# Optimization experiments

Hardware: AMD Instinct MI355X
Metric: run time of the kernel (lower is better)

The kernel has to match this reference:

```python
import jax, jax.numpy as jnp
import numpy as np

N_HEAD, D_MODEL, D_HEAD = 16, 1024, 64
SCALE = 1.0 / (D_HEAD ** 0.5)
LN_EPS = 1e-5


def _rel_shift(x):
    # x: [b, n, i, j] -> Transformer-XL relative shift
    b, n, i, j = x.shape
    zero_pad = jnp.zeros((b, n, i, 1), x.dtype)
    x_padded = jnp.concatenate([zero_pad, x], axis=3).reshape(b, n, j + 1, i)
    return x_padded[:, :, 1:, :].reshape(b, n, i, j)


def setup_inputs() -> dict:
    key = jax.random.key(0)
    ks = jax.random.split(key, 16)
    qlen, bsz, mem_len = 1024, 2, 1024
    klen = qlen + mem_len
    rlen = klen
    s = 0.02
    inp = {
        'w': jax.random.normal(ks[0], (qlen, bsz, D_MODEL), jnp.float32),
        'r': jax.random.normal(ks[1], (rlen, D_MODEL), jnp.float32),
        'mems': jax.random.normal(ks[2], (mem_len, bsz, D_MODEL), jnp.float32),
        'r_w_bias': s * jax.random.normal(ks[3], (N_HEAD, D_HEAD), jnp.float32),
        'r_r_bias': s * jax.random.normal(ks[4], (N_HEAD, D_HEAD), jnp.float32),
        # causal mask with memory offset: position i attends to j <= i + mem_len
        'attn_mask': jnp.triu(jnp.ones((qlen, klen), bool), k=1 + mem_len),
        'Wq': s * jax.random.normal(ks[5], (D_MODEL, N_HEAD * D_HEAD), jnp.float32),
        'bq': jnp.zeros((N_HEAD * D_HEAD,), jnp.float32),
        'Wk': s * jax.random.normal(ks[6], (D_MODEL, N_HEAD * D_HEAD), jnp.float32),
        'bk': jnp.zeros((N_HEAD * D_HEAD,), jnp.float32),
        'Wv': s * jax.random.normal(ks[7], (D_MODEL, N_HEAD * D_HEAD), jnp.float32),
        'bv': jnp.zeros((N_HEAD * D_HEAD,), jnp.float32),
        'Wr': s * jax.random.normal(ks[8], (D_MODEL, N_HEAD * D_HEAD), jnp.float32),
        'br': jnp.zeros((N_HEAD * D_HEAD,), jnp.float32),
        'Wo': s * jax.random.normal(ks[9], (N_HEAD * D_HEAD, D_MODEL), jnp.float32),
        'bo': jnp.zeros((D_MODEL,), jnp.float32),
        'ln_g': jnp.ones((D_MODEL,), jnp.float32),
        'ln_b': jnp.zeros((D_MODEL,), jnp.float32),
    }
    return inp


def reference(w, r, mems, r_w_bias, r_r_bias, Wq, bq, Wk, bk, Wv, bv, Wr, br, Wo, bo, ln_g, ln_b, attn_mask):
    qlen, bsz, _ = w.shape
    cat = jnp.concatenate([mems, w], axis=0)                      # [klen, b, d_model]
    klen = cat.shape[0]
    q = (cat @ Wq + bq)[-qlen:].reshape(qlen, bsz, N_HEAD, D_HEAD)
    k = (cat @ Wk + bk).reshape(klen, bsz, N_HEAD, D_HEAD)
    v = (cat @ Wv + bv).reshape(klen, bsz, N_HEAD, D_HEAD)
    rk = (r @ Wr + br).reshape(-1, N_HEAD, D_HEAD)               # [rlen, n, d]

    AC = jnp.einsum('ibnd,jbnd->bnij', q + r_w_bias, k)          # content term
    BD = _rel_shift(jnp.einsum('ibnd,jnd->bnij', q + r_r_bias, rk))  # relative term
    attn_score = SCALE * (AC + BD)                                # [b, n, i, j]
    attn_score = jnp.where(attn_mask[None, None, :, :], -jnp.inf, attn_score)
    attn_prob = jax.nn.softmax(attn_score, axis=3)
    attn_vec = jnp.einsum('bnij,jbnd->ibnd', attn_prob, v).reshape(qlen, bsz, N_HEAD * D_HEAD)
    attn_out = attn_vec @ Wo + bo

    res = w + attn_out                                            # post-LN (pre_lnorm=False)
    mu = jnp.mean(res, axis=-1, keepdims=True)
    var = jnp.var(res, axis=-1, keepdims=True)
    return (res - mu) / jnp.sqrt(var + LN_EPS) * ln_g + ln_b
```

## Files before the change

kernel.cpp:

```cpp
#include <hip/hip_runtime.h>
#include <math.h>

#define N_HEADC 16
#define D_MODELC 1024
#define D_HEADC 64
#define QLENC 1024
#define BSZC 2
#define MEMLENC 1024
#define KLENC 2048
#define SCALEC 0.125f
#define SL2C 0.18033688011112042f
#define LN_EPSC 1e-5f
#define RINGC 192

typedef __attribute__((ext_vector_type(8))) short short8;
typedef __attribute__((ext_vector_type(4))) float f32x4;

#define MFMA16(a, b, c) __builtin_amdgcn_mfma_f32_16x16x32_bf16((a), (b), (c), 0, 0, 0)

__device__ inline unsigned short f2bf(float x) {
    union { float f; unsigned int u; } c; c.f = x;
    unsigned int r = c.u + 0x7FFFu + ((c.u >> 16) & 1u);
    return (unsigned short)(r >> 16);
}
__device__ inline unsigned int pk2(float a, float b) {
    union { float f; unsigned int u; } x, y; x.f = a; y.f = b;
    return (x.u >> 16) | (y.u & 0xFFFF0000u);
}
__device__ inline float bf2f(short s) {
    union { unsigned int u; float f; } c; c.u = ((unsigned int)(unsigned short)s) << 16;
    return c.f;
}

__device__ __forceinline__ void load_lds16(const short* g, short* l) {
    __builtin_amdgcn_global_load_lds(
        (const __attribute__((address_space(1))) void*)g,
        (__attribute__((address_space(3))) void*)l,
        16, 0, 0);
}

__global__ __launch_bounds__(256) void cast_cat_kernel(
    const float* __restrict__ s0, const float* __restrict__ s1, int splitElems,
    short* __restrict__ dst)
{
    int idx = (blockIdx.x * 256 + threadIdx.x) * 8;
    const float* src = (idx < splitElems) ? (s0 + idx) : (s1 + (idx - splitElems));
    short8 o;
    #pragma unroll
    for (int e = 0; e < 8; ++e) o[e] = (short)f2bf(src[e]);
    *(short8*)(dst + idx) = o;
}

__global__ __launch_bounds__(256) void tcast5_kernel(
    const float* __restrict__ W0, const float* __restrict__ W1,
    const float* __restrict__ W2, const float* __restrict__ W3,
    const float* __restrict__ W4,
    short* __restrict__ D0, short* __restrict__ D1, short* __restrict__ D2,
    short* __restrict__ D3, short* __restrict__ D4)
{
    __shared__ short tile[64][72];
    const float* W; short* D;
    switch (blockIdx.z) {
        case 0: W = W0; D = D0; break;
        case 1: W = W1; D = D1; break;
        case 2: W = W2; D = D2; break;
        case 3: W = W3; D = D3; break;
        default: W = W4; D = D4; break;
    }
    const int t = threadIdx.x;
    const int n0 = blockIdx.x * 64, k0 = blockIdx.y * 64;
    #pragma unroll
    for (int it = 0; it < 2; ++it) {
        int idx = t + it * 256;
        int kl = idx >> 3, c8 = idx & 7;
        const float* src = W + (size_t)(k0 + kl) * D_MODELC + n0 + c8 * 8;
        short8 s;
        #pragma unroll
        for (int e = 0; e < 8; ++e) s[e] = (short)f2bf(src[e]);
        *(short8*)&tile[kl][c8 * 8] = s;
    }
    __syncthreads();
    #pragma unroll
    for (int it = 0; it < 2; ++it) {
        int idx = t + it * 256;
        int nl = idx >> 3, c8 = idx & 7;
        short8 s;
        #pragma unroll
        for (int e = 0; e < 8; ++e) s[e] = tile[c8 * 8 + e][nl];
        *(short8*)(D + (size_t)(n0 + nl) * D_MODELC + k0 + c8 * 8) = s;
    }
}

__global__ __launch_bounds__(256) void vtrans_kernel(
    const short* __restrict__ v_bf, short* __restrict__ vt)
{
    __shared__ short tile[64][72];
    const int t = threadIdx.x;
    const int j0 = blockIdx.x * 64;
    const int bn = blockIdx.y;
    const int b = bn & 1, n = bn >> 1;
    #pragma unroll
    for (int it = 0; it < 2; ++it) {
        int idx = t + it * 256;
        int jl = idx >> 3, c8 = idx & 7;
        short8 s = *(const short8*)(v_bf + ((size_t)(j0 + jl) * 2 + b) * D_MODELC + n * 64 + c8 * 8);
        *(short8*)&tile[jl][c8 * 8] = s;
    }
    __syncthreads();
    #pragma unroll
    for (int it = 0; it < 2; ++it) {
        int idx = t + it * 256;
        int dl = idx >> 3, c8 = idx & 7;
        short8 s;
        #pragma unroll
        for (int e = 0; e < 8; ++e) s[e] = tile[c8 * 8 + e][dl];
        *(short8*)(vt + ((size_t)(b * 16 + n) * 64 + dl) * (size_t)KLENC + j0 + c8 * 8) = s;
    }
}

__global__ __launch_bounds__(256, 3) void proj_gemm_kernel(
    const short* __restrict__ cat, const short* __restrict__ rin,
    const short* __restrict__ WqT, const short* __restrict__ WkT,
    const short* __restrict__ WvT, const short* __restrict__ WrT,
    const float* __restrict__ bq, const float* __restrict__ bk,
    const float* __restrict__ bv, const float* __restrict__ br,
    const float* __restrict__ rwb, const float* __restrict__ rrb,
    short* __restrict__ qw, short* __restrict__ qr,
    short* __restrict__ kb, short* __restrict__ vb, short* __restrict__ rk)
{
    __shared__ short As[3][128][32];
    __shared__ short Bs[3][128][32];

    const int lin = blockIdx.y * 8 + blockIdx.x;
    const int sw  = (lin & 7) * 96 + (lin >> 3);
    const int bx  = sw & 7;
    const int by  = sw >> 3;

    const short* A; const short* Bt; const float* bias; int yt, mode;
    if (by < 32)      { A = cat;                         Bt = WkT; bias = bk; yt = by;      mode = 0; }
    else if (by < 64) { A = cat;                         Bt = WvT; bias = bv; yt = by - 32; mode = 1; }
    else if (by < 80) { A = cat + (size_t)2048 * 1024;   Bt = WqT; bias = bq; yt = by - 64; mode = 2; }
    else              { A = rin;                         Bt = WrT; bias = br; yt = by - 80; mode = 3; }

    const int row0 = yt * 128, col0 = bx * 128;
    const int t = threadIdx.x;
    const int lane = t & 63, wid = t >> 6;
    const int row16 = lane & 15, g8 = lane >> 4;
    const int wr = wid >> 1, wc = wid & 1;

    f32x4 acc[4][4];
    #pragma unroll
    for (int m = 0; m < 4; ++m)
        #pragma unroll
        for (int nn = 0; nn < 4; ++nn)
            acc[m][nn] = (f32x4){0.f, 0.f, 0.f, 0.f};

    const int srow4 = lane >> 2;
    const int cs4 = (lane & 3) ^ ((lane >> 3) & 3);
    const short* Ag = A  + (size_t)(row0 + wid * 32 + srow4) * D_MODELC + cs4 * 8;
    const short* Bg = Bt + (size_t)(col0 + wid * 32 + srow4) * D_MODELC + cs4 * 8;
    const int xc2 = (row16 >> 1) & 3;

    #pragma unroll
    for (int pb = 0; pb < 2; ++pb) {
        int k0 = pb * 32;
        load_lds16(Ag + k0,             &As[pb][0][0] + wid * 1024);
        load_lds16(Ag + k0 + 16 * 1024, &As[pb][0][0] + wid * 1024 + 512);
        load_lds16(Bg + k0,             &Bs[pb][0][0] + wid * 1024);
        load_lds16(Bg + k0 + 16 * 1024, &Bs[pb][0][0] + wid * 1024 + 512);
    }
    asm volatile("s_waitcnt vmcnt(4)" ::: "memory");
    __builtin_amdgcn_s_barrier();

    for (int kk = 0; kk < 32; ++kk) {
        int kpre = (kk + 2 <= 31) ? (kk + 2) * 32 : 31 * 32;
        int bpre = (kk + 2) % 3;
        load_lds16(Ag + kpre,             &As[bpre][0][0] + wid * 1024);
        load_lds16(Ag + kpre + 16 * 1024, &As[bpre][0][0] + wid * 1024 + 512);
        load_lds16(Bg + kpre,             &Bs[bpre][0][0] + wid * 1024);
        load_lds16(Bg + kpre + 16 * 1024, &Bs[bpre][0][0] + wid * 1024 + 512);

        const int bc = kk % 3;
        short8 af[4], bfr[4];
        #pragma unroll
        for (int m = 0; m < 4; ++m)
            af[m] = *(const short8*)&As[bc][wr * 64 + m * 16 + row16][(g8 ^ xc2) * 8];
        #pragma unroll
        for (int nn = 0; nn < 4; ++nn)
            bfr[nn] = *(const short8*)&Bs[bc][wc * 64 + nn * 16 + row16][(g8 ^ xc2) * 8];
        __builtin_amdgcn_s_setprio(1);
        #pragma unroll
        for (int m = 0; m < 4; ++m)
            #pragma unroll
            for (int nn = 0; nn < 4; ++nn)
                acc[m][nn] = MFMA16(af[m], bfr[nn], acc[m][nn]);
        __builtin_amdgcn_s_setprio(0);

        asm volatile("s_waitcnt vmcnt(4)" ::: "memory");
        __builtin_amdgcn_s_barrier();
    }
    asm volatile("s_waitcnt vmcnt(0)" ::: "memory");

    float bvv[4], w1[4], w2[4];
    #pragma unroll
    for (int nn = 0; nn < 4; ++nn) {
        int c = col0 + wc * 64 + nn * 16 + row16;
        bvv[nn] = bias[c];
        w1[nn] = rwb[c];
        w2[nn] = rrb[c];
    }
    if (mode == 2) {
        #pragma unroll
        for (int m = 0; m < 4; ++m)
            #pragma unroll
            for (int nn = 0; nn < 4; ++nn) {
                int c = col0 + wc * 64 + nn * 16 + row16;
                #pragma unroll
                for (int reg = 0; reg < 4; ++reg) {
                    int r = row0 + wr * 64 + m * 16 + g8 * 4 + reg;
                    float v = acc[m][nn][reg] + bvv[nn];
                    qw[(size_t)r * D_MODELC + c] = (short)f2bf((v + w1[nn]) * SL2C);
                    qr[(size_t)r * D_MODELC + c] = (short)f2bf((v + w2[nn]) * SL2C);
                }
            }
    } else {
        short* C = (mode == 0) ? kb : (mode == 1) ? vb : rk;
        #pragma unroll
        for (int m = 0; m < 4; ++m)
            #pragma unroll
            for (int nn = 0; nn < 4; ++nn) {
                int c = col0 + wc * 64 + nn * 16 + row16;
                #pragma unroll
                for (int reg = 0; reg < 4; ++reg) {
                    int r = row0 + wr * 64 + m * 16 + g8 * 4 + reg;
                    C[(size_t)r * D_MODELC + c] = (short)f2bf(acc[m][nn][reg] + bvv[nn]);
                }
            }
    }
}

__global__ __launch_bounds__(256, 3) void wo_gemm_kernel(
    const short* __restrict__ A, const short* __restrict__ Bt,
    float* __restrict__ out0, float* __restrict__ out1)
{
    __shared__ short As[3][128][32];
    __shared__ short Bs[3][128][32];
    const int kz = blockIdx.z;
    float* C = kz ? out1 : out0;
    const int row0 = blockIdx.y * 128, col0 = blockIdx.x * 128;
    const int t = threadIdx.x;
    const int lane = t & 63, wid = t >> 6;
    const int row16 = lane & 15, g8 = lane >> 4;
    const int wr = wid >> 1, wc = wid & 1;

    f32x4 acc[4][4];
    #pragma unroll
    for (int m = 0; m < 4; ++m)
        #pragma unroll
        for (int nn = 0; nn < 4; ++nn)
            acc[m][nn] = (f32x4){0.f, 0.f, 0.f, 0.f};

    const int srow4 = lane >> 2;
    const int cs4 = (lane & 3) ^ ((lane >> 3) & 3);
    const int kbase = kz * 512;
    const short* Ag = A  + (size_t)(row0 + wid * 32 + srow4) * D_MODELC + kbase + cs4 * 8;
    const short* Bg = Bt + (size_t)(col0 + wid * 32 + srow4) * D_MODELC + kbase + cs4 * 8;
    const int xc2 = (row16 >> 1) & 3;

    #pragma unroll
    for (int pb = 0; pb < 2; ++pb) {
        int k0 = pb * 32;
        load_lds16(Ag + k0,             &As[pb][0][0] + wid * 1024);
        load_lds16(Ag + k0 + 16 * 1024, &As[pb][0][0] + wid * 1024 + 512);
        load_lds16(Bg + k0,             &Bs[pb][0][0] + wid * 1024);
        load_lds16(Bg + k0 + 16 * 1024, &Bs[pb][0][0] + wid * 1024 + 512);
    }
    asm volatile("s_waitcnt vmcnt(4)" ::: "memory");
    __builtin_amdgcn_s_barrier();

    for (int kk = 0; kk < 16; ++kk) {
        int kpre = (kk + 2 <= 15) ? (kk + 2) * 32 : 15 * 32;
        int bpre = (kk + 2) % 3;
        load_lds16(Ag + kpre,             &As[bpre][0][0] + wid * 1024);
        load_lds16(Ag + kpre + 16 * 1024, &As[bpre][0][0] + wid * 1024 + 512);
        load_lds16(Bg + kpre,             &Bs[bpre][0][0] + wid * 1024);
        load_lds16(Bg + kpre + 16 * 1024, &Bs[bpre][0][0] + wid * 1024 + 512);

        const int bc = kk % 3;
        short8 af[4], bfr[4];
        #pragma unroll
        for (int m = 0; m < 4; ++m)
            af[m] = *(const short8*)&As[bc][wr * 64 + m * 16 + row16][(g8 ^ xc2) * 8];
        #pragma unroll
        for (int nn = 0; nn < 4; ++nn)
            bfr[nn] = *(const short8*)&Bs[bc][wc * 64 + nn * 16 + row16][(g8 ^ xc2) * 8];
        __builtin_amdgcn_s_setprio(1);
        #pragma unroll
        for (int m = 0; m < 4; ++m)
            #pragma unroll
            for (int nn = 0; nn < 4; ++nn)
                acc[m][nn] = MFMA16(af[m], bfr[nn], acc[m][nn]);
        __builtin_amdgcn_s_setprio(0);

        asm volatile("s_waitcnt vmcnt(4)" ::: "memory");
        __builtin_amdgcn_s_barrier();
    }
    asm volatile("s_waitcnt vmcnt(0)" ::: "memory");

    #pragma unroll
    for (int m = 0; m < 4; ++m)
        #pragma unroll
        for (int nn = 0; nn < 4; ++nn) {
            int c = col0 + wc * 64 + nn * 16 + row16;
            #pragma unroll
            for (int reg = 0; reg < 4; ++reg) {
                int r = row0 + wr * 64 + m * 16 + g8 * 4 + reg;
                C[(size_t)r * D_MODELC + c] = acc[m][nn][reg];
            }
        }
}

__global__ __launch_bounds__(256, 2) void attn_mfma_kernel(
    const short* __restrict__ qw, const short* __restrict__ qr,
    const short* __restrict__ kb, const short* __restrict__ rkb,
    const short* __restrict__ vt, short* __restrict__ av)
{
    __shared__ short Kl[2][64][64];
    __shared__ short Vl[3][64][64];
    __shared__ short Rl[RINGC][64];
    __shared__ short pun[4][1376];
    __shared__ float scb[4][16];

    const int wave = threadIdx.x >> 6, lane = threadIdx.x & 63;
    const int row16 = lane & 15, g8 = lane >> 4;
    const int srow = lane >> 3, chk = lane & 7;
    const int swz = srow & 7;

    const int lin = blockIdx.y * 16 + blockIdx.x;
    const int xcd = lin & 7;
    const int u   = lin >> 3;
    const int v   = u & 31;
    const int bn  = xcd * 4 + (v >> 3);
    const int tt  = v & 7;
    const int ic  = (u >> 5) ? (15 - tt) : tt;
    const int b = bn & 1, n = bn >> 1;
    const int i0 = ic * 64;
    const int i0w = i0 + wave * 16;

    short8 qwf[2], qrf[2];
    #pragma unroll
    for (int ks = 0; ks < 2; ++ks) {
        size_t off = ((size_t)(i0w + row16) * 2 + b) * D_MODELC + n * 64 + ks * 32 + g8 * 8;
        qwf[ks] = *(const short8*)(qw + off);
        qrf[ks] = *(const short8*)(qr + off);
    }

    #pragma unroll
    for (int t = 0; t < 2; ++t) {
        int rr = wave * 16 + t * 8;
        int j  = rr + srow;
        int cs = chk ^ swz;
        load_lds16(kb + ((size_t)j * 2 + b) * D_MODELC + n * 64 + cs * 8, &Kl[0][rr][0]);
        load_lds16(vt + ((size_t)((b * 16 + n) * 64 + rr + srow)) * KLENC + cs * 8,
                   &Vl[0][rr][0]);
    }
    {
        const int p0 = 960 - i0;
        #pragma unroll
        for (int t = 0; t < 4; ++t) {
            int jrb_ = p0 + wave * 32 + t * 8;
            int slotb = jrb_ % RINGC;
            int jr = jrb_ + srow;
            int jc = jr < KLENC ? jr : KLENC - 1;
            int cs = chk ^ swz;
            load_lds16(rkb + (size_t)jc * D_MODELC + n * 64 + cs * 8, &Rl[slotb][0]);
        }
    }

    f32x4 accO[4];
    #pragma unroll
    for (int dt = 0; dt < 4; ++dt) accO[dt] = (f32x4){0.f, 0.f, 0.f, 0.f};
    float m = -INFINITY, lsum = 0.f;

    const int T = (i0 + 63 + MEMLENC + 64) >> 6;
    const int r7 = row16 & 7;

    __syncthreads();

    int cur = 0;
    int vp = 2, vc = 0, vn = 1;
    for (int s = 0; s < T; ++s) {
        const int j0 = s * 64;
        const int nxt = cur ^ 1;

        #pragma unroll
        for (int t = 0; t < 2; ++t) {
            int rr = wave * 16 + t * 8;
            int j  = j0 + 64 + rr + srow;
            if (j > KLENC - 1) j = KLENC - 1;
            int cs = chk ^ swz;
            load_lds16(kb + ((size_t)j * 2 + b) * D_MODELC + n * 64 + cs * 8, &Kl[nxt][rr][0]);
        }
        {
            const int nb = j0 + 1088 - i0;
            #pragma unroll
            for (int t = 0; t < 2; ++t) {
                int jrb_ = nb + wave * 16 + t * 8;
                int slotb = jrb_ % RINGC;
                int jr = jrb_ + srow;
                int jc = jr < KLENC ? jr : KLENC - 1;
                int cs = chk ^ swz;
                load_lds16(rkb + (size_t)jc * D_MODELC + n * 64 + cs * 8, &Rl[slotb][0]);
            }
        }
        {
            const int jsrc = (j0 + 64 <= KLENC - 64) ? (j0 + 64) : (KLENC - 64);
            #pragma unroll
            for (int t = 0; t < 2; ++t) {
                int rr = wave * 16 + t * 8;
                int cs = chk ^ swz;
                load_lds16(vt + ((size_t)((b * 16 + n) * 64 + rr + srow)) * KLENC + jsrc + cs * 8,
                           &Vl[vn][rr][0]);
            }
        }

        short* pP  = &pun[wave][0];
        short* bdT = &pun[wave][0];

        __builtin_amdgcn_s_setprio(1);
        f32x4 st[4];
        #pragma unroll
        for (int jt = 0; jt < 4; ++jt) {
            st[jt] = (f32x4){0.f, 0.f, 0.f, 0.f};
            const short* kr = &Kl[cur][jt * 16 + row16][0];
            st[jt] = MFMA16(*(const short8*)(kr + ((g8 ^ r7) * 8)),       qwf[0], st[jt]);
            st[jt] = MFMA16(*(const short8*)(kr + (((4 + g8) ^ r7) * 8)), qwf[1], st[jt]);
        }

        if (s) {
            #pragma unroll
            for (int ks2 = 0; ks2 < 2; ++ks2) {
                short8 pf = *(const short8*)&pP[row16 * 64 + (((ks2 * 4 + g8) ^ r7) * 8)];
                #pragma unroll
                for (int dt = 0; dt < 4; ++dt) {
                    const short* vpp = &Vl[vp][dt * 16 + row16][(((ks2 * 4 + g8) ^ r7) * 8)];
                    accO[dt] = MFMA16(pf, *(const short8*)vpp, accO[dt]);
                }
            }
        }

        const int jrb_w = j0 - i0w + 1008;
        const int sb = jrb_w % RINGC;
        #pragma unroll
        for (int rt = 0; rt < 5; ++rt) {
            int rsl = sb + rt * 16 + row16;
            if (rsl >= RINGC) rsl -= RINGC;
            const short* rr = &Rl[rsl][0];
            f32x4 bd = (f32x4){0.f, 0.f, 0.f, 0.f};
            bd = MFMA16(*(const short8*)(rr + ((g8 ^ r7) * 8)),       qrf[0], bd);
            bd = MFMA16(*(const short8*)(rr + (((4 + g8) ^ r7) * 8)), qrf[1], bd);
            uint2 wv;
            wv.x = pk2(bd[0], bd[1]);
            wv.y = pk2(bd[2], bd[3]);
            *(uint2*)&bdT[row16 * 84 + rt * 16 + g8 * 4] = wv;
        }
        __builtin_amdgcn_s_setprio(0);

        float sl[4][4];
        if (j0 + 63 <= i0w + MEMLENC) {
            #pragma unroll
            for (int jt = 0; jt < 4; ++jt)
                #pragma unroll
                for (int reg = 0; reg < 4; ++reg) {
                    const int jl = jt * 16 + g8 * 4 + reg;
                    sl[jt][reg] = st[jt][reg] + bf2f(bdT[row16 * 84 + jl + 15 - row16]);
                }
        } else {
            #pragma unroll
            for (int jt = 0; jt < 4; ++jt)
                #pragma unroll
                for (int reg = 0; reg < 4; ++reg) {
                    const int jl = jt * 16 + g8 * 4 + reg;
                    float vv = st[jt][reg] + bf2f(bdT[row16 * 84 + jl + 15 - row16]);
                    sl[jt][reg] = (j0 + jl > i0w + row16 + MEMLENC) ? -INFINITY : vv;
                }
        }

        float mx0 = fmaxf(fmaxf(sl[0][0], sl[0][1]), fmaxf(sl[0][2], sl[0][3]));
        float mx1 = fmaxf(fmaxf(sl[1][0], sl[1][1]), fmaxf(sl[1][2], sl[1][3]));
        float mx2 = fmaxf(fmaxf(sl[2][0], sl[2][1]), fmaxf(sl[2][2], sl[2][3]));
        float mx3 = fmaxf(fmaxf(sl[3][0], sl[3][1]), fmaxf(sl[3][2], sl[3][3]));
        float mx = fmaxf(fmaxf(mx0, mx1), fmaxf(mx2, mx3));
        mx = fmaxf(mx, __shfl_xor(mx, 16, 64));
        mx = fmaxf(mx, __shfl_xor(mx, 32, 64));

        if (__any(mx > m + 8.f)) {
            float mn = fmaxf(m, mx);
            float sc = exp2f(m - mn);
            m = mn;
            lsum *= sc;
            if (lane < 16) scb[wave][lane] = sc;
            float4 s4 = *(const float4*)&scb[wave][g8 * 4];
            #pragma unroll
            for (int dt = 0; dt < 4; ++dt) {
                accO[dt][0] *= s4.x; accO[dt][1] *= s4.y;
                accO[dt][2] *= s4.z; accO[dt][3] *= s4.w;
            }
        }

        #pragma unroll
        for (int jt = 0; jt < 4; ++jt)
            #pragma unroll
            for (int reg = 0; reg < 4; ++reg)
                sl[jt][reg] = exp2f(sl[jt][reg] - m);
        float ps = ((sl[0][0] + sl[0][1]) + (sl[0][2] + sl[0][3]))
                 + ((sl[1][0] + sl[1][1]) + (sl[1][2] + sl[1][3]))
                 + ((sl[2][0] + sl[2][1]) + (sl[2][2] + sl[2][3]))
                 + ((sl[3][0] + sl[3][1]) + (sl[3][2] + sl[3][3]));
        #pragma unroll
        for (int jt = 0; jt < 4; ++jt) {
            const int ch = (jt * 2 + (g8 >> 1)) ^ r7;
            uint2 pkd;
            pkd.x = pk2(sl[jt][0], sl[jt][1]);
            pkd.y = pk2(sl[jt][2], sl[jt][3]);
            *(uint2*)&pP[row16 * 64 + ch * 8 + (g8 & 1) * 4] = pkd;
        }
        ps += __shfl_xor(ps, 16, 64);
        ps += __shfl_xor(ps, 32, 64);
        lsum += ps;

        __syncthreads();
        cur = nxt;
        int tmp = vp; vp = vc; vc = vn; vn = tmp;
    }

    {
        short* pP = &pun[wave][0];
        #pragma unroll
        for (int ks2 = 0; ks2 < 2; ++ks2) {
            short8 pf = *(const short8*)&pP[row16 * 64 + (((ks2 * 4 + g8) ^ r7) * 8)];
            #pragma unroll
            for (int dt = 0; dt < 4; ++dt) {
                const short* vpp = &Vl[vp][dt * 16 + row16][(((ks2 * 4 + g8) ^ r7) * 8)];
                accO[dt] = MFMA16(pf, *(const short8*)vpp, accO[dt]);
            }
        }
    }

    if (lane < 16) scb[wave][lane] = lsum;
    float4 l4 = *(const float4*)&scb[wave][g8 * 4];
    float rl4[4] = {1.f / l4.x, 1.f / l4.y, 1.f / l4.z, 1.f / l4.w};
    #pragma unroll
    for (int dt = 0; dt < 4; ++dt)
        #pragma unroll
        for (int reg = 0; reg < 4; ++reg) {
            size_t o = ((size_t)(i0w + g8 * 4 + reg) * 2 + b) * D_MODELC + n * 64 + dt * 16 + row16;
            av[o] = (short)f2bf(accO[dt][reg] * rl4[reg]);
        }
}

__global__ __launch_bounds__(256) void ln_kernel(
    const float* __restrict__ w, const float* __restrict__ ao0,
    const float* __restrict__ ao1, const float* __restrict__ bo,
    const float* __restrict__ g, const float* __restrict__ bb,
    float* __restrict__ out)
{
    __shared__ float red[2][4];
    const int row = blockIdx.x;
    const int lane = threadIdx.x & 63;
    const int wv = threadIdx.x >> 6;
    const size_t base = (size_t)row * D_MODELC;
    const int c = threadIdx.x * 4;

    float4 xw = *(const float4*)&w[base + c];
    float4 x0 = *(const float4*)&ao0[base + c];
    float4 x1 = *(const float4*)&ao1[base + c];
    float4 xb = *(const float4*)&bo[c];
    float x[4] = {xw.x + x0.x + x1.x + xb.x, xw.y + x0.y + x1.y + xb.y,
                  xw.z + x0.z + x1.z + xb.z, xw.w + x0.w + x1.w + xb.w};

    float sum = x[0] + x[1] + x[2] + x[3];
    float ssq = x[0]*x[0] + x[1]*x[1] + x[2]*x[2] + x[3]*x[3];
    #pragma unroll
    for (int off = 32; off > 0; off >>= 1) {
        sum += __shfl_xor(sum, off, 64);
        ssq += __shfl_xor(ssq, off, 64);
    }
    if (lane == 0) { red[0][wv] = sum; red[1][wv] = ssq; }
    __syncthreads();
    sum = red[0][0] + red[0][1] + red[0][2] + red[0][3];
    ssq = red[1][0] + red[1][1] + red[1][2] + red[1][3];

    const float mu = sum * (1.0f / D_MODELC);
    const float var = ssq * (1.0f / D_MODELC) - mu * mu;
    const float rstd = rsqrtf(var + LN_EPSC);

    float4 o;
    o.x = (x[0] - mu) * rstd * g[c] + bb[c];
    o.y = (x[1] - mu) * rstd * g[c+1] + bb[c+1];
    o.z = (x[2] - mu) * rstd * g[c+2] + bb[c+2];
    o.w = (x[3] - mu) * rstd * g[c+3] + bb[c+3];
    *(float4*)&out[base + c] = o;
}

extern "C" void kernel_launch(void* const* d_in, const int* in_sizes, int n_in,
                              void* d_out, int out_size, void* d_ws, size_t ws_size,
                              hipStream_t stream)
{
    const float* w    = (const float*)d_in[0];
    const float* r    = (const float*)d_in[1];
    const float* mems = (const float*)d_in[2];
    const float* rwb  = (const float*)d_in[3];
    const float* rrb  = (const float*)d_in[4];
    const float* Wq = (const float*)d_in[6];
    const float* bq = (const float*)d_in[7];
    const float* Wk = (const float*)d_in[8];
    const float* bk = (const float*)d_in[9];
    const float* Wv = (const float*)d_in[10];
    const float* bv = (const float*)d_in[11];
    const float* Wr = (const float*)d_in[12];
    const float* br = (const float*)d_in[13];
    const float* Wo = (const float*)d_in[14];
    const float* bo = (const float*)d_in[15];
    const float* ln_g = (const float*)d_in[16];
    const float* ln_b = (const float*)d_in[17];
    float* out = (float*)d_out;

    char* ws = (char*)d_ws;
    const size_t MB = 1ull << 20;
    short* cat_bf = (short*)(ws + 0 * MB);
    short* r_bf   = (short*)(ws + 8 * MB);
    short* Wq_t   = (short*)(ws + 12 * MB);
    short* Wk_t   = (short*)(ws + 14 * MB);
    short* Wv_t   = (short*)(ws + 16 * MB);
    short* Wr_t   = (short*)(ws + 18 * MB);
    short* Wo_t   = (short*)(ws + 20 * MB);
    short* qw_bf  = (short*)(ws + 22 * MB);
    short* qr_bf  = (short*)(ws + 26 * MB);
    short* k_bf   = (short*)(ws + 30 * MB);
    short* v_bf   = (short*)(ws + 38 * MB);
    short* rk_bf  = (short*)(ws + 46 * MB);
    short* vt     = (short*)(ws + 50 * MB);
    short* av_bf  = (short*)(ws + 58 * MB);
    float* ao0    = (float*)v_bf;
    float* ao1    = (float*)k_bf;

    dim3 blk(256);

    cast_cat_kernel<<<dim3(2048), blk, 0, stream>>>(mems, w, 2048 * 1024, cat_bf);
    cast_cat_kernel<<<dim3(1024), blk, 0, stream>>>(r, r, 1 << 30, r_bf);

    tcast5_kernel<<<dim3(16, 16, 5), blk, 0, stream>>>(
        Wq, Wk, Wv, Wr, Wo, Wq_t, Wk_t, Wv_t, Wr_t, Wo_t);

    proj_gemm_kernel<<<dim3(8, 96), blk, 0, stream>>>(
        cat_bf, r_bf, Wq_t, Wk_t, Wv_t, Wr_t,
        bq, bk, bv, br, rwb, rrb,
        qw_bf, qr_bf, k_bf, v_bf, rk_bf);

    vtrans_kernel<<<dim3(32, 32), blk, 0, stream>>>(v_bf, vt);

    attn_mfma_kernel<<<dim3(16, 32), blk, 0, stream>>>(
        qw_bf, qr_bf, k_bf, rk_bf, vt, av_bf);

    wo_gemm_kernel<<<dim3(8, 16, 2), blk, 0, stream>>>(av_bf, Wo_t, ao0, ao1);

    ln_kernel<<<dim3(2048), blk, 0, stream>>>(w, ao0, ao1, bo, ln_g, ln_b, out);
}
```

Baseline: 159.3 us.

## Split attention KV range across two blocks with merge kernel, bf16 Wo partials

Each attention block now handles every other 64-key tile (split by parity jh), which doubles the grid to 16x64 and raises occupancy on the causal-imbalanced workload. Unnormalized partial outputs are stored in bf16 together with the running max and sum, and a new merge kernel combines the two halves. The P·V MFMA is moved in-iteration instead of being software-pipelined one step behind, and the R ring is enlarged to a power of two so a mask replaces the modulo. Wo GEMM partials are also written as bf16 instead of fp32 to cut traffic into LayerNorm, at some precision cost and with an extra launch.

```diff
diff --git a/kernel.cpp b/kernel.cpp
--- a/kernel.cpp
+++ b/kernel.cpp
@@ -11,7 +11,7 @@
 #define SCALEC 0.125f
 #define SL2C 0.18033688011112042f
 #define LN_EPSC 1e-5f
-#define RINGC 192
+#define RINGC 256
 
 typedef __attribute__((ext_vector_type(8))) short short8;
 typedef __attribute__((ext_vector_type(4))) float f32x4;
@@ -241,12 +241,12 @@
 
 __global__ __launch_bounds__(256, 3) void wo_gemm_kernel(
     const short* __restrict__ A, const short* __restrict__ Bt,
-    float* __restrict__ out0, float* __restrict__ out1)
+    short* __restrict__ out0, short* __restrict__ out1)
 {
     __shared__ short As[3][128][32];
     __shared__ short Bs[3][128][32];
     const int kz = blockIdx.z;
-    float* C = kz ? out1 : out0;
+    short* C = kz ? out1 : out0;
     const int row0 = blockIdx.y * 128, col0 = blockIdx.x * 128;
     const int t = threadIdx.x;
     const int lane = t & 63, wid = t >> 6;
@@ -315,7 +315,7 @@
             #pragma unroll
             for (int reg = 0; reg < 4; ++reg) {
                 int r = row0 + wr * 64 + m * 16 + g8 * 4 + reg;
-                C[(size_t)r * D_MODELC + c] = acc[m][nn][reg];
+                C[(size_t)r * D_MODELC + c] = (short)f2bf(acc[m][nn][reg]);
             }
         }
 }
@@ -323,10 +323,11 @@
 __global__ __launch_bounds__(256, 2) void attn_mfma_kernel(
     const short* __restrict__ qw, const short* __restrict__ qr,
     const short* __restrict__ kb, const short* __restrict__ rkb,
-    const short* __restrict__ vt, short* __restrict__ av)
+    const short* __restrict__ vt,
+    short* __restrict__ Op0, short* __restrict__ Op1, float* __restrict__ ml)
 {
     __shared__ short Kl[2][64][64];
-    __shared__ short Vl[3][64][64];
+    __shared__ short Vl[2][64][64];
     __shared__ short Rl[RINGC][64];
     __shared__ short pun[4][1376];
     __shared__ float scb[4][16];
@@ -339,10 +340,10 @@
     const int lin = blockIdx.y * 16 + blockIdx.x;
     const int xcd = lin & 7;
     const int u   = lin >> 3;
-    const int v   = u & 31;
-    const int bn  = xcd * 4 + (v >> 3);
-    const int tt  = v & 7;
-    const int ic  = (u >> 5) ? (15 - tt) : tt;
+    const int bn  = xcd * 4 + (u & 3);
+    const int rest = u >> 2;
+    const int ic  = rest & 15;
+    const int jh  = rest >> 4;
     const int b = bn & 1, n = bn >> 1;
     const int i0 = ic * 64;
     const int i0w = i0 + wave * 16;
@@ -355,25 +356,26 @@
         qrf[ks] = *(const short8*)(qr + off);
     }
 
+    const int j00 = jh * 64;
     #pragma unroll
     for (int t = 0; t < 2; ++t) {
         int rr = wave * 16 + t * 8;
-        int j  = rr + srow;
         int cs = chk ^ swz;
-        load_lds16(kb + ((size_t)j * 2 + b) * D_MODELC + n * 64 + cs * 8, &Kl[0][rr][0]);
-        load_lds16(vt + ((size_t)((b * 16 + n) * 64 + rr + srow)) * KLENC + cs * 8,
+        load_lds16(kb + ((size_t)(j00 + rr + srow) * 2 + b) * D_MODELC + n * 64 + cs * 8,
+                   &Kl[0][rr][0]);
+        load_lds16(vt + ((size_t)((b * 16 + n) * 64 + rr + srow)) * KLENC + j00 + cs * 8,
                    &Vl[0][rr][0]);
     }
     {
-        const int p0 = 960 - i0;
+        const int p0 = j00 + 960 - i0;
         #pragma unroll
         for (int t = 0; t < 4; ++t) {
             int jrb_ = p0 + wave * 32 + t * 8;
-            int slotb = jrb_ % RINGC;
+            int slot = jrb_ & (RINGC - 1);
             int jr = jrb_ + srow;
             int jc = jr < KLENC ? jr : KLENC - 1;
             int cs = chk ^ swz;
-            load_lds16(rkb + (size_t)jc * D_MODELC + n * 64 + cs * 8, &Rl[slotb][0]);
+            load_lds16(rkb + (size_t)jc * D_MODELC + n * 64 + cs * 8, &Rl[slot][0]);
         }
     }
 
@@ -388,15 +390,14 @@
     __syncthreads();
 
     int cur = 0;
-    int vp = 2, vc = 0, vn = 1;
-    for (int s = 0; s < T; ++s) {
+    for (int s = jh; s < T; s += 2) {
         const int j0 = s * 64;
         const int nxt = cur ^ 1;
 
         #pragma unroll
         for (int t = 0; t < 2; ++t) {
             int rr = wave * 16 + t * 8;
-            int j  = j0 + 64 + rr + srow;
+            int j  = j0 + 128 + rr + srow;
             if (j > KLENC - 1) j = KLENC - 1;
             int cs = chk ^ swz;
             load_lds16(kb + ((size_t)j * 2 + b) * D_MODELC + n * 64 + cs * 8, &Kl[nxt][rr][0]);
@@ -404,28 +405,25 @@
         {
             const int nb = j0 + 1088 - i0;
             #pragma unroll
-            for (int t = 0; t < 2; ++t) {
-                int jrb_ = nb + wave * 16 + t * 8;
-                int slotb = jrb_ % RINGC;
+            for (int t = 0; t < 4; ++t) {
+                int jrb_ = nb + wave * 32 + t * 8;
+                int slot = jrb_ & (RINGC - 1);
                 int jr = jrb_ + srow;
                 int jc = jr < KLENC ? jr : KLENC - 1;
                 int cs = chk ^ swz;
-                load_lds16(rkb + (size_t)jc * D_MODELC + n * 64 + cs * 8, &Rl[slotb][0]);
+                load_lds16(rkb + (size_t)jc * D_MODELC + n * 64 + cs * 8, &Rl[slot][0]);
             }
         }
         {
-            const int jsrc = (j0 + 64 <= KLENC - 64) ? (j0 + 64) : (KLENC - 64);
+            const int jsrc = (j0 + 128 <= KLENC - 64) ? (j0 + 128) : (KLENC - 64);
             #pragma unroll
             for (int t = 0; t < 2; ++t) {
                 int rr = wave * 16 + t * 8;
                 int cs = chk ^ swz;
                 load_lds16(vt + ((size_t)((b * 16 + n) * 64 + rr + srow)) * KLENC + jsrc + cs * 8,
-                           &Vl[vn][rr][0]);
+                           &Vl[nxt][rr][0]);
             }
         }
-
-        short* pP  = &pun[wave][0];
-        short* bdT = &pun[wave][0];
 
         __builtin_amdgcn_s_setprio(1);
         f32x4 st[4];
@@ -437,24 +435,11 @@
             st[jt] = MFMA16(*(const short8*)(kr + (((4 + g8) ^ r7) * 8)), qwf[1], st[jt]);
         }
 
-        if (s) {
-            #pragma unroll
-            for (int ks2 = 0; ks2 < 2; ++ks2) {
-                short8 pf = *(const short8*)&pP[row16 * 64 + (((ks2 * 4 + g8) ^ r7) * 8)];
-                #pragma unroll
-                for (int dt = 0; dt < 4; ++dt) {
-                    const short* vpp = &Vl[vp][dt * 16 + row16][(((ks2 * 4 + g8) ^ r7) * 8)];
-                    accO[dt] = MFMA16(pf, *(const short8*)vpp, accO[dt]);
-                }
-            }
-        }
-
         const int jrb_w = j0 - i0w + 1008;
-        const int sb = jrb_w % RINGC;
+        short* bdT = &pun[wave][0];
         #pragma unroll
         for (int rt = 0; rt < 5; ++rt) {
-            int rsl = sb + rt * 16 + row16;
-            if (rsl >= RINGC) rsl -= RINGC;
+            int rsl = (jrb_w + rt * 16 + row16) & (RINGC - 1);
             const short* rr = &Rl[rsl][0];
             f32x4 bd = (f32x4){0.f, 0.f, 0.f, 0.f};
             bd = MFMA16(*(const short8*)(rr + ((g8 ^ r7) * 8)),       qrf[0], bd);
@@ -517,6 +502,7 @@
                  + ((sl[1][0] + sl[1][1]) + (sl[1][2] + sl[1][3]))
                  + ((sl[2][0] + sl[2][1]) + (sl[2][2] + sl[2][3]))
                  + ((sl[3][0] + sl[3][1]) + (sl[3][2] + sl[3][3]));
+        short* pP = &pun[wave][0];
         #pragma unroll
         for (int jt = 0; jt < 4; ++jt) {
             const int ch = (jt * 2 + (g8 >> 1)) ^ r7;
@@ -529,39 +515,55 @@
         ps += __shfl_xor(ps, 32, 64);
         lsum += ps;
 
+        __builtin_amdgcn_s_setprio(1);
+        #pragma unroll
+        for (int ks2 = 0; ks2 < 2; ++ks2) {
+            short8 pf = *(const short8*)&pP[row16 * 64 + (((ks2 * 4 + g8) ^ r7) * 8)];
+            #pragma unroll
+            for (int dt = 0; dt < 4; ++dt) {
+                const short* vpp = &Vl[cur][dt * 16 + row16][(((ks2 * 4 + g8) ^ r7) * 8)];
+                accO[dt] = MFMA16(pf, *(const short8*)vpp, accO[dt]);
+            }
+        }
+        __builtin_amdgcn_s_setprio(0);
+
         __syncthreads();
         cur = nxt;
-        int tmp = vp; vp = vc; vc = vn; vn = tmp;
-    }
-
-    {
-        short* pP = &pun[wave][0];
-        #pragma unroll
-        for (int ks2 = 0; ks2 < 2; ++ks2) {
-            short8 pf = *(const short8*)&pP[row16 * 64 + (((ks2 * 4 + g8) ^ r7) * 8)];
-            #pragma unroll
-            for (int dt = 0; dt < 4; ++dt) {
-                const short* vpp = &Vl[vp][dt * 16 + row16][(((ks2 * 4 + g8) ^ r7) * 8)];
-                accO[dt] = MFMA16(pf, *(const short8*)vpp, accO[dt]);
-            }
-        }
-    }
-
-    if (lane < 16) scb[wave][lane] = lsum;
-    float4 l4 = *(const float4*)&scb[wave][g8 * 4];
-    float rl4[4] = {1.f / l4.x, 1.f / l4.y, 1.f / l4.z, 1.f / l4.w};
+    }
+
+    short* Op = jh ? Op1 : Op0;
     #pragma unroll
     for (int dt = 0; dt < 4; ++dt)
         #pragma unroll
         for (int reg = 0; reg < 4; ++reg) {
-            size_t o = ((size_t)(i0w + g8 * 4 + reg) * 2 + b) * D_MODELC + n * 64 + dt * 16 + row16;
-            av[o] = (short)f2bf(accO[dt][reg] * rl4[reg]);
-        }
+            int g = ((i0w + g8 * 4 + reg) * 2 + b) * 16 + n;
+            Op[(size_t)g * 64 + dt * 16 + row16] = (short)f2bf(accO[dt][reg]);
+        }
+    if (g8 == 0) {
+        int g = ((i0w + row16) * 2 + b) * 16 + n;
+        ml[jh * 65536 + g]         = m;
+        ml[jh * 65536 + 32768 + g] = lsum;
+    }
+}
+
+__global__ __launch_bounds__(256) void attn_merge_kernel(
+    const short* __restrict__ Op0, const short* __restrict__ Op1,
+    const float* __restrict__ ml, short* __restrict__ av)
+{
+    const int g = blockIdx.x * 4 + (threadIdx.x >> 6);
+    const int d = threadIdx.x & 63;
+    float m0 = ml[g],         l0 = ml[32768 + g];
+    float m1 = ml[65536 + g], l1 = ml[98304 + g];
+    float M  = fmaxf(m0, m1);
+    float e0 = exp2f(m0 - M), e1 = exp2f(m1 - M);
+    float rden = 1.f / (l0 * e0 + l1 * e1);
+    size_t o = (size_t)g * 64 + d;
+    av[o] = (short)f2bf((bf2f(Op0[o]) * e0 + bf2f(Op1[o]) * e1) * rden);
 }
 
 __global__ __launch_bounds__(256) void ln_kernel(
-    const float* __restrict__ w, const float* __restrict__ ao0,
-    const float* __restrict__ ao1, const float* __restrict__ bo,
+    const float* __restrict__ w, const short* __restrict__ p0,
+    const short* __restrict__ p1, const float* __restrict__ bo,
     const float* __restrict__ g, const float* __restrict__ bb,
     float* __restrict__ out)
 {
@@ -573,11 +575,13 @@
     const int c = threadIdx.x * 4;
 
     float4 xw = *(const float4*)&w[base + c];
-    float4 x0 = *(const float4*)&ao0[base + c];
-    float4 x1 = *(const float4*)&ao1[base + c];
+    ushort4 a0 = *(const ushort4*)&p0[base + c];
+    ushort4 a1 = *(const ushort4*)&p1[base + c];
     float4 xb = *(const float4*)&bo[c];
-    float x[4] = {xw.x + x0.x + x1.x + xb.x, xw.y + x0.y + x1.y + xb.y,
-                  xw.z + x0.z + x1.z + xb.z, xw.w + x0.w + x1.w + xb.w};
+    float x[4] = {xw.x + bf2f((short)a0.x) + bf2f((short)a1.x) + xb.x,
+                  xw.y + bf2f((short)a0.y) + bf2f((short)a1.y) + xb.y,
+                  xw.z + bf2f((short)a0.z) + bf2f((short)a1.z) + xb.z,
+                  xw.w + bf2f((short)a0.w) + bf2f((short)a1.w) + xb.w};
 
     float sum = x[0] + x[1] + x[2] + x[3];
     float ssq = x[0]*x[0] + x[1]*x[1] + x[2]*x[2] + x[3]*x[3];
@@ -642,8 +646,11 @@
     short* rk_bf  = (short*)(ws + 46 * MB);
     short* vt     = (short*)(ws + 50 * MB);
     short* av_bf  = (short*)(ws + 58 * MB);
-    float* ao0    = (float*)v_bf;
-    float* ao1    = (float*)k_bf;
+    short* Op0    = cat_bf;
+    short* Op1    = (short*)(ws + 4 * MB);
+    float* mlp    = (float*)r_bf;
+    short* wo0    = Wq_t;
+    short* wo1    = Wv_t;
 
     dim3 blk(256);
 
@@ -660,10 +667,12 @@
 
     vtrans_kernel<<<dim3(32, 32), blk, 0, stream>>>(v_bf, vt);
 
-    attn_mfma_kernel<<<dim3(16, 32), blk, 0, stream>>>(
-        qw_bf, qr_bf, k_bf, rk_bf, vt, av_bf);
-
-    wo_gemm_kernel<<<dim3(8, 16, 2), blk, 0, stream>>>(av_bf, Wo_t, ao0, ao1);
-
-    ln_kernel<<<dim3(2048), blk, 0, stream>>>(w, ao0, ao1, bo, ln_g, ln_b, out);
-}
+    attn_mfma_kernel<<<dim3(16, 64), blk, 0, stream>>>(
+        qw_bf, qr_bf, k_bf, rk_bf, vt, Op0, Op1, mlp);
+
+    attn_merge_kernel<<<dim3(8192), blk, 0, stream>>>(Op0, Op1, mlp, av_bf);
+
+    wo_gemm_kernel<<<dim3(8, 16, 2), blk, 0, stream>>>(av_bf, Wo_t, wo0, wo1);
+
+    ln_kernel<<<dim3(2048), blk, 0, stream>>>(w, wo0, wo1, bo, ln_g, ln_b, out);
+}
```

Result: slower. 166.5 us (+4.5%).
